# Kernel optimization log

Hardware: AMD Instinct MI355X
Metric: run time of the kernel (lower is better)

Reference implementation:

```python
import jax, jax.numpy as jnp
import numpy as np

B, S, D, H = 4, 2048, 768, 12
HD = D // H  # head_dim = 64

def setup_inputs() -> dict:
    key = jax.random.key(0)
    k1, k2, k3 = jax.random.split(key, 3)
    scale = 0.02
    return {
        "x": jax.random.normal(k1, (B, S, D), dtype=jnp.float32),
        "w_qkv": jax.random.normal(k2, (D, 3 * D), dtype=jnp.float32) * scale,
        "b_qkv": jnp.zeros((3 * D,), dtype=jnp.float32),
        "w_proj": jax.random.normal(k3, (D, D), dtype=jnp.float32) * scale,
        "b_proj": jnp.zeros((D,), dtype=jnp.float32),
    }

def reference(x, w_qkv, b_qkv, w_proj, b_proj):
    b, s, d = x.shape
    hd = d // H
    attn_scale = hd ** -0.5
    qkv = x @ w_qkv + b_qkv                      # [b, s, 3d]
    qkv = qkv.reshape(b, s, 3, H, hd)
    q, k, v = jnp.moveaxis(qkv, 2, 0)            # each [b, s, H, hd]
    q = q.transpose(0, 2, 1, 3)                  # [b, H, s, hd]
    k = k.transpose(0, 2, 1, 3)
    v = v.transpose(0, 2, 1, 3)
    attn = jnp.einsum("bhqd,bhkd->bhqk", q, k) * attn_scale  # [b, H, s, s]
    causal = jnp.tril(jnp.ones((s, s), dtype=bool))
    attn = jnp.where(causal[None, None], attn, -jnp.inf)
    attn = jax.nn.softmax(attn, axis=-1)
    out = jnp.einsum("bhqk,bhkd->bhqd", attn, v)  # [b, H, s, hd]
    out = out.transpose(0, 2, 1, 3).reshape(b, s, d)
    return out @ w_proj + b_proj
```

## Files before the change

kernel.cpp:

```cpp
#include <hip/hip_runtime.h>
#include <hip/hip_bf16.h>
#include <cstdint>

typedef __bf16 bf16_t;
typedef __bf16 bf16x4 __attribute__((ext_vector_type(4)));
typedef __bf16 bf16x8 __attribute__((ext_vector_type(8)));
typedef float floatx4 __attribute__((ext_vector_type(4)));
typedef float floatx16 __attribute__((ext_vector_type(16)));
typedef unsigned int u32x4 __attribute__((ext_vector_type(4)));

#define NB 4
#define NH 12
#define SEQ 2048
#define DM 768
#define LOG2E 1.44269504088896340736f

__device__ __forceinline__ void gload_lds16(const bf16_t* g, bf16_t* l) {
  auto gp = reinterpret_cast<const __attribute__((address_space(1))) uint32_t*>(
      reinterpret_cast<uintptr_t>(g));
  auto lp = reinterpret_cast<__attribute__((address_space(3))) uint32_t*>(
      reinterpret_cast<uintptr_t>(l));
  __builtin_amdgcn_global_load_lds(gp, lp, 16, 0, 0);
}

__device__ __forceinline__ unsigned int pack2(float a, float b) {
  bf16_t x = (bf16_t)a, y = (bf16_t)b;
  unsigned short ux = __builtin_bit_cast(unsigned short, x);
  unsigned short uy = __builtin_bit_cast(unsigned short, y);
  return (unsigned int)ux | ((unsigned int)uy << 16);
}

__global__ __launch_bounds__(256) void cvt_kernel(const float* __restrict__ in,
                                                  bf16_t* __restrict__ out) {
  int i = (blockIdx.x * 256 + threadIdx.x) * 4;
  float4 v = *(const float4*)(in + i);
  bf16x4 h;
  h[0] = (bf16_t)v.x; h[1] = (bf16_t)v.y; h[2] = (bf16_t)v.z; h[3] = (bf16_t)v.w;
  *(bf16x4*)(out + i) = h;
}

__global__ __launch_bounds__(256) void transpose_cvt_kernel(const float* __restrict__ in,
                                                            bf16_t* __restrict__ out,
                                                            int K, int N) {
  __shared__ float tile[32][33];
  int nb = blockIdx.x * 32, kb = blockIdx.y * 32;
  int tx = threadIdx.x & 31, ty = threadIdx.x >> 5;
#pragma unroll
  for (int r = ty; r < 32; r += 8)
    tile[r][tx] = in[(size_t)(kb + r) * N + nb + tx];
  __syncthreads();
#pragma unroll
  for (int r = ty; r < 32; r += 8)
    out[(size_t)(nb + r) * K + kb + tx] = (bf16_t)tile[tx][r];
}

__global__ __launch_bounds__(256) void gemm_qkv_kernel(
    const bf16_t* __restrict__ A, const bf16_t* __restrict__ BT,
    const float* __restrict__ bias,
    bf16_t* __restrict__ Qo, bf16_t* __restrict__ Ko, bf16_t* __restrict__ Vo) {
  const int K = 768;
  __shared__ __align__(16) bf16_t As[128][32];
  __shared__ __align__(16) bf16_t Bs[128][32];
  const int m0 = blockIdx.x * 128, n0 = blockIdx.y * 128;
  const int tid = threadIdx.x;
  const int w = tid >> 6, lane = tid & 63, quad = lane >> 4, l16 = lane & 15;
  const int wm = w >> 1, wn = w & 1;
  const int ldrow = w * 32;
  const int grow = lane >> 2;
  const int gcol = (lane & 3) * 8;

  floatx4 acc[4][4];
#pragma unroll
  for (int mt = 0; mt < 4; mt++)
#pragma unroll
    for (int nt = 0; nt < 4; nt++) acc[mt][nt] = (floatx4)(0.f);

  const bf16_t* ga0 = A + (size_t)(m0 + ldrow) * K;
  const bf16_t* gb0 = BT + (size_t)(n0 + ldrow) * K;

  for (int k0 = 0; k0 < K; k0 += 32) {
    __syncthreads();
    gload_lds16(ga0 + (size_t)grow * K + k0 + gcol,        &As[ldrow][0]);
    gload_lds16(ga0 + (size_t)(grow + 16) * K + k0 + gcol, &As[ldrow + 16][0]);
    gload_lds16(gb0 + (size_t)grow * K + k0 + gcol,        &Bs[ldrow][0]);
    gload_lds16(gb0 + (size_t)(grow + 16) * K + k0 + gcol, &Bs[ldrow + 16][0]);
    __syncthreads();
    bf16x8 af[4], bfr[4];
#pragma unroll
    for (int mt = 0; mt < 4; mt++)
      af[mt] = *(const bf16x8*)&As[wm * 64 + mt * 16 + l16][quad * 8];
#pragma unroll
    for (int nt = 0; nt < 4; nt++)
      bfr[nt] = *(const bf16x8*)&Bs[wn * 64 + nt * 16 + l16][quad * 8];
#pragma unroll
    for (int mt = 0; mt < 4; mt++)
#pragma unroll
      for (int nt = 0; nt < 4; nt++)
        acc[mt][nt] = __builtin_amdgcn_mfma_f32_16x16x32_bf16(af[mt], bfr[nt], acc[mt][nt], 0, 0, 0);
  }

  const int which = n0 / 768;
  const int rem0 = n0 % 768;
  bf16_t* dst = which == 0 ? Qo : (which == 1 ? Ko : Vo);
  const float qscale = which == 0 ? (0.125f * LOG2E) : 1.0f;
#pragma unroll
  for (int nt = 0; nt < 4; nt++) {
    const int cc = wn * 64 + nt * 16 + l16;
    const int rem = rem0 + cc;
    const int h = rem >> 6, hd = rem & 63;
    const float bv = bias[n0 + cc];
#pragma unroll
    for (int mt = 0; mt < 4; mt++)
#pragma unroll
      for (int r = 0; r < 4; r++) {
        const int gr = m0 + wm * 64 + mt * 16 + quad * 4 + r;
        const int bb = gr >> 11, s = gr & 2047;
        const float val = (acc[mt][nt][r] + bv) * qscale;
        dst[((size_t)((bb * NH + h) * SEQ + s)) * 64 + hd] = (bf16_t)val;
      }
  }
}

__global__ __launch_bounds__(256) void vtrans_kernel(const bf16_t* __restrict__ V,
                                                     bf16_t* __restrict__ Vt) {
  __shared__ bf16_t tile[64][66];
  int bh = blockIdx.y, s0 = blockIdx.x * 64;
  int tid = threadIdx.x;
  int r = tid >> 4, c4 = (tid & 15) * 4;
  const bf16_t* src = V + (size_t)bh * SEQ * 64;
#pragma unroll
  for (int rr = r; rr < 64; rr += 16)
    *(bf16x4*)&tile[rr][c4] = *(const bf16x4*)&src[(size_t)(s0 + rr) * 64 + c4];
  __syncthreads();
  bf16_t* dst = Vt + (size_t)bh * 64 * SEQ;
#pragma unroll
  for (int hd = r; hd < 64; hd += 16) {
    bf16x4 o;
    o[0] = tile[c4 + 0][hd]; o[1] = tile[c4 + 1][hd];
    o[2] = tile[c4 + 2][hd]; o[3] = tile[c4 + 3][hd];
    *(bf16x4*)&dst[(size_t)hd * SEQ + s0 + c4] = o;
  }
}

__global__ __launch_bounds__(256, 3) void attn_kernel(
    const bf16_t* __restrict__ Q, const bf16_t* __restrict__ Kg,
    const bf16_t* __restrict__ Vt, bf16_t* __restrict__ Out) {
  __shared__ __align__(16) bf16_t Ks[3][64 * 64];
  __shared__ __align__(16) bf16_t Vs[3][64 * 64];
  const int tid = threadIdx.x;
  const int w = tid >> 6, lane = tid & 63;
  const int l31 = lane & 31, hi = lane >> 5;
  const int bh = blockIdx.x;
  const int b = bh / NH, h = bh % NH;
  const int qt = (int)(gridDim.y - 1) - (int)blockIdx.y;
  const int r0 = qt * 128 + w * 32;
  const int qrow = r0 + l31;
  const bf16_t* Qp = Q + (size_t)bh * SEQ * 64;
  const bf16_t* Kp = Kg + (size_t)bh * SEQ * 64;
  const bf16_t* Vp = Vt + (size_t)bh * 64 * SEQ;

  bf16x8 qf[4];
#pragma unroll
  for (int kc = 0; kc < 4; kc++)
    qf[kc] = *(const bf16x8*)&Qp[(size_t)qrow * 64 + kc * 16 + hi * 8];

  bf16x8 ones;
#pragma unroll
  for (int j = 0; j < 8; j++) ones[j] = (bf16_t)1.0f;

  float m_i = -1e30f;
  floatx16 accT[2];
  accT[0] = (floatx16)(0.f);
  accT[1] = (floatx16)(0.f);
  floatx16 zl = (floatx16)(0.f);

  const int nt_w = (r0 >> 6) + 1;
  const int ntmax = 2 * qt + 2;

  int srow[2], scolb[2];
#pragma unroll
  for (int r = 0; r < 2; r++) {
    int off = r * 4096 + w * 1024 + lane * 16;
    int row = off >> 7;
    srow[r] = row;
    scolb[r] = (off & 127) ^ ((row & 7) << 4);
  }

  auto stage = [&](int buf, int kt) {
    const int kbase = kt * 64;
#pragma unroll
    for (int r = 0; r < 2; r++) {
      gload_lds16(Kp + (size_t)(kbase + srow[r]) * 64 + (scolb[r] >> 1),
                  &Ks[buf][r * 2048 + w * 512]);
      gload_lds16(Vp + (size_t)srow[r] * SEQ + kbase + (scolb[r] >> 1),
                  &Vs[buf][r * 2048 + w * 512]);
    }
  };

  const int swz = (l31 & 7) << 4;

  stage(0, 0);

  int cur = 0;
  for (int kt = 0; kt < ntmax; kt++) {
    const int nxt = (cur == 2) ? 0 : cur + 1;
    if (kt + 1 < ntmax) {
      stage(nxt, kt + 1);
      asm volatile("s_waitcnt vmcnt(4)" ::: "memory");
    } else {
      asm volatile("s_waitcnt vmcnt(0)" ::: "memory");
    }
    __builtin_amdgcn_s_barrier();

    if (kt < nt_w) {
      const int kbase = kt * 64;
      const bf16_t* Kb = Ks[cur];
      const bf16_t* Vb = Vs[cur];
      floatx16 st[2];
#pragma unroll
      for (int kt2 = 0; kt2 < 2; kt2++) {
        const int row = kt2 * 32 + l31;
        floatx16 z = (floatx16)(0.f);
#pragma unroll
        for (int kc = 0; kc < 4; kc++) {
          bf16x8 kfr = *(const bf16x8*)&Kb[row * 64 + (((kc * 32 + hi * 16) ^ swz) >> 1)];
          z = __builtin_amdgcn_mfma_f32_32x32x16_bf16(kfr, qf[kc], z, 0, 0, 0);
        }
        st[kt2] = z;
      }
      if (kt == nt_w - 1) {
#pragma unroll
        for (int kt2 = 0; kt2 < 2; kt2++)
#pragma unroll
          for (int r = 0; r < 16; r++) {
            int key = kbase + kt2 * 32 + (r & 3) + 8 * (r >> 2) + 4 * hi;
            if (key > qrow) st[kt2][r] = -1e30f;
          }
      }
      float mloc = -1e30f;
#pragma unroll
      for (int kt2 = 0; kt2 < 2; kt2++)
#pragma unroll
        for (int r = 0; r < 16; r++) mloc = fmaxf(mloc, st[kt2][r]);
      mloc = fmaxf(mloc, __shfl_xor(mloc, 32));
      if (!__all((int)(mloc - m_i <= 8.f))) {
        const float mnew = fmaxf(m_i, mloc);
        const float al = __builtin_amdgcn_exp2f(m_i - mnew);
        m_i = mnew;
#pragma unroll
        for (int r = 0; r < 16; r++) zl[r] *= al;
#pragma unroll
        for (int dt = 0; dt < 2; dt++)
#pragma unroll
          for (int r = 0; r < 16; r++) accT[dt][r] *= al;
      }
#pragma unroll
      for (int kt2 = 0; kt2 < 2; kt2++)
#pragma unroll
        for (int r = 0; r < 16; r++)
          st[kt2][r] = __builtin_amdgcn_exp2f(st[kt2][r] - m_i);
#pragma unroll
      for (int kt2 = 0; kt2 < 2; kt2++) {
        unsigned int wds[8];
#pragma unroll
        for (int j = 0; j < 8; j++) wds[j] = pack2(st[kt2][2 * j], st[kt2][2 * j + 1]);
        unsigned int x0 = (unsigned int)__shfl_xor((int)(hi ? wds[0] : wds[2]), 32);
        unsigned int x1 = (unsigned int)__shfl_xor((int)(hi ? wds[1] : wds[3]), 32);
        unsigned int x2 = (unsigned int)__shfl_xor((int)(hi ? wds[4] : wds[6]), 32);
        unsigned int x3 = (unsigned int)__shfl_xor((int)(hi ? wds[5] : wds[7]), 32);
        u32x4 f0 = hi ? (u32x4){x0, x1, wds[2], wds[3]} : (u32x4){wds[0], wds[1], x0, x1};
        u32x4 f1 = hi ? (u32x4){x2, x3, wds[6], wds[7]} : (u32x4){wds[4], wds[5], x2, x3};
        bf16x8 pf0 = __builtin_bit_cast(bf16x8, f0);
        bf16x8 pf1 = __builtin_bit_cast(bf16x8, f1);
        zl = __builtin_amdgcn_mfma_f32_32x32x16_bf16(ones, pf0, zl, 0, 0, 0);
        zl = __builtin_amdgcn_mfma_f32_32x32x16_bf16(ones, pf1, zl, 0, 0, 0);
#pragma unroll
        for (int dt = 0; dt < 2; dt++) {
          const int vrow = dt * 32 + l31;
          bf16x8 v0 = *(const bf16x8*)&Vb[vrow * 64 + (((kt2 * 64 + hi * 16) ^ swz) >> 1)];
          bf16x8 v1 = *(const bf16x8*)&Vb[vrow * 64 + (((kt2 * 64 + 32 + hi * 16) ^ swz) >> 1)];
          accT[dt] = __builtin_amdgcn_mfma_f32_32x32x16_bf16(v0, pf0, accT[dt], 0, 0, 0);
          accT[dt] = __builtin_amdgcn_mfma_f32_32x32x16_bf16(v1, pf1, accT[dt], 0, 0, 0);
        }
      }
    }
    cur = nxt;
  }

  const float inv_l = 1.0f / zl[0];
#pragma unroll
  for (int dt = 0; dt < 2; dt++)
#pragma unroll
    for (int g = 0; g < 4; g++) {
      bf16x4 o;
#pragma unroll
      for (int j = 0; j < 4; j++) o[j] = (bf16_t)(accT[dt][4 * g + j] * inv_l);
      int d = dt * 32 + 8 * g + 4 * hi;
      *(bf16x4*)&Out[((size_t)(b * SEQ + qrow)) * DM + h * 64 + d] = o;
    }
}

__global__ __launch_bounds__(256) void gemm_proj_kernel(
    const bf16_t* __restrict__ A, const bf16_t* __restrict__ BT,
    const float* __restrict__ bias, float* __restrict__ out) {
  const int K = 768;
  __shared__ __align__(16) bf16_t As[128][32];
  __shared__ __align__(16) bf16_t Bs[128][32];
  const int m0 = blockIdx.x * 128, n0 = blockIdx.y * 128;
  const int tid = threadIdx.x;
  const int w = tid >> 6, lane = tid & 63, quad = lane >> 4, l16 = lane & 15;
  const int wm = w >> 1, wn = w & 1;
  const int ldrow = w * 32;
  const int grow = lane >> 2;
  const int gcol = (lane & 3) * 8;

  floatx4 acc[4][4];
#pragma unroll
  for (int mt = 0; mt < 4; mt++)
#pragma unroll
    for (int nt = 0; nt < 4; nt++) acc[mt][nt] = (floatx4)(0.f);

  const bf16_t* ga0 = A + (size_t)(m0 + ldrow) * K;
  const bf16_t* gb0 = BT + (size_t)(n0 + ldrow) * K;

  for (int k0 = 0; k0 < K; k0 += 32) {
    __syncthreads();
    gload_lds16(ga0 + (size_t)grow * K + k0 + gcol,        &As[ldrow][0]);
    gload_lds16(ga0 + (size_t)(grow + 16) * K + k0 + gcol, &As[ldrow + 16][0]);
    gload_lds16(gb0 + (size_t)grow * K + k0 + gcol,        &Bs[ldrow][0]);
    gload_lds16(gb0 + (size_t)(grow + 16) * K + k0 + gcol, &Bs[ldrow + 16][0]);
    __syncthreads();
    bf16x8 af[4], bfr[4];
#pragma unroll
    for (int mt = 0; mt < 4; mt++)
      af[mt] = *(const bf16x8*)&As[wm * 64 + mt * 16 + l16][quad * 8];
#pragma unroll
    for (int nt = 0; nt < 4; nt++)
      bfr[nt] = *(const bf16x8*)&Bs[wn * 64 + nt * 16 + l16][quad * 8];
#pragma unroll
    for (int mt = 0; mt < 4; mt++)
#pragma unroll
      for (int nt = 0; nt < 4; nt++)
        acc[mt][nt] = __builtin_amdgcn_mfma_f32_16x16x32_bf16(af[mt], bfr[nt], acc[mt][nt], 0, 0, 0);
  }

#pragma unroll
  for (int nt = 0; nt < 4; nt++) {
    const int gc = n0 + wn * 64 + nt * 16 + l16;
    const float bv = bias[gc];
#pragma unroll
    for (int mt = 0; mt < 4; mt++)
#pragma unroll
      for (int r = 0; r < 4; r++) {
        const int gr = m0 + wm * 64 + mt * 16 + quad * 4 + r;
        out[(size_t)gr * 768 + gc] = acc[mt][nt][r] + bv;
      }
  }
}

extern "C" void kernel_launch(void* const* d_in, const int* in_sizes, int n_in,
                              void* d_out, int out_size, void* d_ws, size_t ws_size,
                              hipStream_t stream) {
  const float* x      = (const float*)d_in[0];
  const float* w_qkv  = (const float*)d_in[1];
  const float* b_qkv  = (const float*)d_in[2];
  const float* w_proj = (const float*)d_in[3];
  const float* b_proj = (const float*)d_in[4];
  float* out = (float*)d_out;
  char* ws = (char*)d_ws;

  bf16_t* xb     = (bf16_t*)(ws + 0);
  bf16_t* wqkvT  = (bf16_t*)(ws + 12582912);
  bf16_t* wprojT = (bf16_t*)(ws + 16121856);
  bf16_t* q      = (bf16_t*)(ws + 17301504);
  bf16_t* k      = (bf16_t*)(ws + 29884416);
  bf16_t* v      = (bf16_t*)(ws + 42467328);
  bf16_t* ao     = (bf16_t*)(ws + 55050240);
  bf16_t* vt     = xb;

  cvt_kernel<<<6144, 256, 0, stream>>>(x, xb);
  transpose_cvt_kernel<<<dim3(72, 24), 256, 0, stream>>>(w_qkv, wqkvT, 768, 2304);
  transpose_cvt_kernel<<<dim3(24, 24), 256, 0, stream>>>(w_proj, wprojT, 768, 768);
  gemm_qkv_kernel<<<dim3(64, 18), 256, 0, stream>>>(xb, wqkvT, b_qkv, q, k, v);
  vtrans_kernel<<<dim3(32, 48), 256, 0, stream>>>(v, vt);
  attn_kernel<<<dim3(48, 16), 256, 0, stream>>>(q, k, vt, ao);
  gemm_proj_kernel<<<dim3(64, 6), 256, 0, stream>>>(ao, wprojT, b_proj, out);
}
```

Baseline: 208.8 us.

## Fuse prep conversions into one kernel and double attention query tile to 256 rows

The three conversion launches (x cast, two weight transpose-casts) are merged into one prep kernel that picks its job from the block index. The attention kernel now runs 512 threads (8 waves) per block covering 256 query rows. Each K/V tile staged in LDS is therefore shared by twice as many waves, and each thread issues one load per tensor per tile, with the vmcnt wait adjusted to match. The trade-off is half as many attention blocks (384), coarser causal load balance, and a larger idle share for early waves in the diagonal tiles.

```diff
diff --git a/kernel.cpp b/kernel.cpp
--- a/kernel.cpp
+++ b/kernel.cpp
@@ -30,21 +30,35 @@
   return (unsigned int)ux | ((unsigned int)uy << 16);
 }
 
-__global__ __launch_bounds__(256) void cvt_kernel(const float* __restrict__ in,
-                                                  bf16_t* __restrict__ out) {
-  int i = (blockIdx.x * 256 + threadIdx.x) * 4;
-  float4 v = *(const float4*)(in + i);
-  bf16x4 h;
-  h[0] = (bf16_t)v.x; h[1] = (bf16_t)v.y; h[2] = (bf16_t)v.z; h[3] = (bf16_t)v.w;
-  *(bf16x4*)(out + i) = h;
-}
-
-__global__ __launch_bounds__(256) void transpose_cvt_kernel(const float* __restrict__ in,
-                                                            bf16_t* __restrict__ out,
-                                                            int K, int N) {
+__global__ __launch_bounds__(256) void prep_kernel(
+    const float* __restrict__ x, bf16_t* __restrict__ xb,
+    const float* __restrict__ wqkv, bf16_t* __restrict__ wqkvT,
+    const float* __restrict__ wproj, bf16_t* __restrict__ wprojT) {
+  const int bid = blockIdx.x;
+  const int tid = threadIdx.x;
+  if (bid < 6144) {
+    int i = (bid * 256 + tid) * 4;
+    float4 v = *(const float4*)(x + i);
+    bf16x4 hh;
+    hh[0] = (bf16_t)v.x; hh[1] = (bf16_t)v.y; hh[2] = (bf16_t)v.z; hh[3] = (bf16_t)v.w;
+    *(bf16x4*)(xb + i) = hh;
+    return;
+  }
+  const float* in;
+  bf16_t* out;
+  int N, nb, kb;
+  if (bid < 7872) {
+    int t = bid - 6144;
+    in = wqkv; out = wqkvT; N = 2304;
+    nb = (t % 72) * 32; kb = (t / 72) * 32;
+  } else {
+    int t = bid - 7872;
+    in = wproj; out = wprojT; N = 768;
+    nb = (t % 24) * 32; kb = (t / 24) * 32;
+  }
+  const int K = 768;
   __shared__ float tile[32][33];
-  int nb = blockIdx.x * 32, kb = blockIdx.y * 32;
-  int tx = threadIdx.x & 31, ty = threadIdx.x >> 5;
+  int tx = tid & 31, ty = tid >> 5;
 #pragma unroll
   for (int r = ty; r < 32; r += 8)
     tile[r][tx] = in[(size_t)(kb + r) * N + nb + tx];
@@ -142,7 +156,7 @@
   }
 }
 
-__global__ __launch_bounds__(256, 3) void attn_kernel(
+__global__ __launch_bounds__(512, 4) void attn_kernel(
     const bf16_t* __restrict__ Q, const bf16_t* __restrict__ Kg,
     const bf16_t* __restrict__ Vt, bf16_t* __restrict__ Out) {
   __shared__ __align__(16) bf16_t Ks[3][64 * 64];
@@ -153,7 +167,7 @@
   const int bh = blockIdx.x;
   const int b = bh / NH, h = bh % NH;
   const int qt = (int)(gridDim.y - 1) - (int)blockIdx.y;
-  const int r0 = qt * 128 + w * 32;
+  const int r0 = qt * 256 + w * 32;
   const int qrow = r0 + l31;
   const bf16_t* Qp = Q + (size_t)bh * SEQ * 64;
   const bf16_t* Kp = Kg + (size_t)bh * SEQ * 64;
@@ -175,26 +189,15 @@
   floatx16 zl = (floatx16)(0.f);
 
   const int nt_w = (r0 >> 6) + 1;
-  const int ntmax = 2 * qt + 2;
-
-  int srow[2], scolb[2];
-#pragma unroll
-  for (int r = 0; r < 2; r++) {
-    int off = r * 4096 + w * 1024 + lane * 16;
-    int row = off >> 7;
-    srow[r] = row;
-    scolb[r] = (off & 127) ^ ((row & 7) << 4);
-  }
+  const int ntmax = 4 * qt + 4;
+
+  const int srow = tid >> 3;
+  const int scolb = ((tid & 7) ^ (srow & 7)) << 4;
 
   auto stage = [&](int buf, int kt) {
     const int kbase = kt * 64;
-#pragma unroll
-    for (int r = 0; r < 2; r++) {
-      gload_lds16(Kp + (size_t)(kbase + srow[r]) * 64 + (scolb[r] >> 1),
-                  &Ks[buf][r * 2048 + w * 512]);
-      gload_lds16(Vp + (size_t)srow[r] * SEQ + kbase + (scolb[r] >> 1),
-                  &Vs[buf][r * 2048 + w * 512]);
-    }
+    gload_lds16(Kp + (size_t)(kbase + srow) * 64 + (scolb >> 1), &Ks[buf][w * 512]);
+    gload_lds16(Vp + (size_t)srow * SEQ + kbase + (scolb >> 1), &Vs[buf][w * 512]);
   };
 
   const int swz = (l31 & 7) << 4;
@@ -206,7 +209,7 @@
     const int nxt = (cur == 2) ? 0 : cur + 1;
     if (kt + 1 < ntmax) {
       stage(nxt, kt + 1);
-      asm volatile("s_waitcnt vmcnt(4)" ::: "memory");
+      asm volatile("s_waitcnt vmcnt(2)" ::: "memory");
     } else {
       asm volatile("s_waitcnt vmcnt(0)" ::: "memory");
     }
@@ -378,11 +381,9 @@
   bf16_t* ao     = (bf16_t*)(ws + 55050240);
   bf16_t* vt     = xb;
 
-  cvt_kernel<<<6144, 256, 0, stream>>>(x, xb);
-  transpose_cvt_kernel<<<dim3(72, 24), 256, 0, stream>>>(w_qkv, wqkvT, 768, 2304);
-  transpose_cvt_kernel<<<dim3(24, 24), 256, 0, stream>>>(w_proj, wprojT, 768, 768);
+  prep_kernel<<<8448, 256, 0, stream>>>(x, xb, w_qkv, wqkvT, w_proj, wprojT);
   gemm_qkv_kernel<<<dim3(64, 18), 256, 0, stream>>>(xb, wqkvT, b_qkv, q, k, v);
   vtrans_kernel<<<dim3(32, 48), 256, 0, stream>>>(v, vt);
-  attn_kernel<<<dim3(48, 16), 256, 0, stream>>>(q, k, vt, ao);
+  attn_kernel<<<dim3(48, 8), 512, 0, stream>>>(q, k, vt, ao);
   gemm_proj_kernel<<<dim3(64, 6), 256, 0, stream>>>(ao, wprojT, b_proj, out);
 }
```

After: 214.5 us. 2.8% more time.
